# Optimization experiments

Hardware: AMD Instinct MI355X
Metric: run time of the kernel (lower is better)

Reference implementation:

```python
import jax, jax.numpy as jnp
import numpy as np

DIM, DK, DV = 1024, 128, 128

def setup_inputs() -> dict:
    key = jax.random.key(0)
    ks = jax.random.split(key, 7)
    X = jax.random.normal(ks[0], (4, 4096, DIM), dtype=jnp.float32)
    s = DIM ** -0.5
    Wq = jax.random.normal(ks[1], (DIM, DK), dtype=jnp.float32) * s
    bq = jnp.zeros((DK,), dtype=jnp.float32)
    Wk = jax.random.normal(ks[2], (DIM, DK), dtype=jnp.float32) * s
    bk = jnp.zeros((DK,), dtype=jnp.float32)
    Wv = jax.random.normal(ks[3], (DIM, DV), dtype=jnp.float32) * s
    bv = jnp.zeros((DV,), dtype=jnp.float32)
    return {"X": X, "Wq": Wq, "bq": bq, "Wk": Wk, "bk": bk, "Wv": Wv, "bv": bv}

def reference(X, Wq, bq, Wk, bk, Wv, bv):
    scale = DK ** -0.5
    q = X @ Wq + bq              # [B, S, dk]
    k = X @ Wk + bk              # [B, S, dk]
    v = X @ Wv + bv              # [B, S, dv]
    attn = jnp.einsum('bqd,bkd->bqk', q, k) * scale  # [B, S, S]
    attn = jax.nn.softmax(attn, axis=-1)
    return jnp.einsum('bqk,bkd->bqd', attn, v)       # [B, S, dv]
```

## Files before the change

### kernel.cpp

```cpp
#include <hip/hip_runtime.h>

#define NB 4
#define SEQ 4096
#define DIMK 1024
#define DKV 128
#define SCALE 0.08838834764831845f

typedef float  f32x4  __attribute__((ext_vector_type(4)));
typedef float  f32x16 __attribute__((ext_vector_type(16)));
typedef _Float16 f16x8 __attribute__((ext_vector_type(8)));

static __device__ __forceinline__ int pkrtz(float a, float b) {
    auto h = __builtin_amdgcn_cvt_pkrtz(a, b);
    return __builtin_bit_cast(int, h);
}

__global__ void prep_wt(const float* __restrict__ Wq, const float* __restrict__ Wk,
                        const float* __restrict__ Wv, _Float16* __restrict__ WT) {
    int tid = blockIdx.x * 256 + threadIdx.x;
    int n  = tid & 127;
    int k  = (tid >> 7) & 1023;
    int w3 = tid >> 17;
    const float* W = (w3 == 0) ? Wq : (w3 == 1) ? Wk : Wv;
    WT[((size_t)w3 * 128 + n) * 1024 + k] = (_Float16)W[(size_t)k * 128 + n];
}

__global__ __launch_bounds__(256) void qkv_proj(
    const float* __restrict__ X,
    const float* __restrict__ bq, const float* __restrict__ bk, const float* __restrict__ bv,
    const _Float16* __restrict__ WT,
    _Float16* __restrict__ Qh, _Float16* __restrict__ Kh, _Float16* __restrict__ VTh) {

    __shared__ __attribute__((aligned(16))) _Float16 WTs[128 * 40];
    const int t = threadIdx.x;
    const int w = t >> 6, l = t & 63;
    const int lrow = l & 15, lg = l >> 4;
    const int w3   = blockIdx.x % 3;
    const int tile = blockIdx.x / 3;
    const int r0 = tile * 64;

    f32x4 acc[8] = {};
    const float* xrow = X + (size_t)(r0 + w * 16 + lrow) * DIMK;
    const _Float16* Wbase = WT + (size_t)w3 * 128 * 1024;

    float4 xc0 = *(const float4*)(xrow + lg * 8);
    float4 xc1 = *(const float4*)(xrow + lg * 8 + 4);

    for (int k0 = 0; k0 < DIMK; k0 += 32) {
        __syncthreads();
        #pragma unroll
        for (int i = 0; i < 2; ++i) {
            int c = t + 256 * i;
            int row = c >> 2, part = c & 3;
            *(int4*)((char*)WTs + row * 80 + part * 16) =
                *(const int4*)(Wbase + (size_t)row * 1024 + k0 + part * 8);
        }
        float4 xn0, xn1;
        if (k0 + 32 < DIMK) {
            xn0 = *(const float4*)(xrow + k0 + 32 + lg * 8);
            xn1 = *(const float4*)(xrow + k0 + 32 + lg * 8 + 4);
        }
        __syncthreads();
        f16x8 a;
        a[0] = (_Float16)xc0.x; a[1] = (_Float16)xc0.y; a[2] = (_Float16)xc0.z; a[3] = (_Float16)xc0.w;
        a[4] = (_Float16)xc1.x; a[5] = (_Float16)xc1.y; a[6] = (_Float16)xc1.z; a[7] = (_Float16)xc1.w;

        #pragma unroll
        for (int n = 0; n < 8; ++n) {
            f16x8 bf = *(const f16x8*)((const char*)WTs + (n * 16 + lrow) * 80 + lg * 16);
            acc[n] = __builtin_amdgcn_mfma_f32_16x16x32_f16(a, bf, acc[n], 0, 0, 0);
        }
        xc0 = xn0; xc1 = xn1;
    }
    const float* bias = (w3 == 0) ? bq : (w3 == 1) ? bk : bv;
    #pragma unroll
    for (int n = 0; n < 8; ++n) {
        int col = n * 16 + lrow;
        float bv_ = bias[col];
        #pragma unroll
        for (int j = 0; j < 4; ++j) {
            int grow = r0 + w * 16 + lg * 4 + j;
            float val = acc[n][j] + bv_;
            if (w3 == 0) {
                Qh[(size_t)grow * DKV + col] = (_Float16)(val * SCALE);
            } else if (w3 == 1) {
                Kh[(size_t)grow * DKV + col] = (_Float16)val;
            } else {
                int b = grow >> 12, sp = grow & 4095;
                VTh[((size_t)b * DKV + col) * SEQ + sp] = (_Float16)val;
            }
        }
    }
}

__global__ __launch_bounds__(256, 2) void attn_kernel(
    const _Float16* __restrict__ Qh, const _Float16* __restrict__ Kh,
    const _Float16* __restrict__ VTh, float* __restrict__ out) {

    __shared__ __attribute__((aligned(16))) char lds[65536];

    const int t = threadIdx.x;
    const int w = t >> 6, l = t & 63;
    const int lq = l & 31;
    const int hi = l >> 5;

    const int work = (blockIdx.x & 7) * 64 + (blockIdx.x >> 3);
    const int b  = work >> 7;
    const int qt = work & 127;
    const int q0 = qt * 32;

    char* Kw = lds + w * 16384;
    char* Vw = Kw + 8192;

    f16x8 qf[8];
    #pragma unroll
    for (int c = 0; c < 8; ++c)
        qf[c] = *(const f16x8*)(Qh + (size_t)(b * SEQ + q0 + lq) * DKV + c * 16 + hi * 8);

    f32x16 o[4] = {};
    float m = -INFINITY, lsum = 0.f;

    const _Float16* Kbase = Kh + (size_t)(b * SEQ + w * 1024) * DKV;
    const _Float16* Vbase = VTh + (size_t)b * DKV * SEQ + w * 1024;

    const int krow = l >> 4, kpart = l & 15;
    const int vdv  = l >> 2, vp = l & 3;

    {
        int4 kreg[8], vreg[8];
        #pragma unroll
        for (int i = 0; i < 8; ++i)
            kreg[i] = *(const int4*)(Kbase + (size_t)(krow + 4 * i) * DKV + kpart * 8);
        #pragma unroll
        for (int i = 0; i < 8; ++i)
            vreg[i] = *(const int4*)(Vbase + (size_t)(vdv + 16 * i) * SEQ + vp * 8);
        #pragma unroll
        for (int i = 0; i < 8; ++i) {
            int row = krow + 4 * i;
            *(int4*)(Kw + row * 256 + ((kpart * 16) ^ ((row & 15) << 4))) = kreg[i];
        }
        #pragma unroll
        for (int i = 0; i < 8; ++i) {
            int dv = vdv + 16 * i;
            *(int4*)(Vw + dv * 64 + ((vp ^ ((dv >> 1) & 3)) * 16)) = vreg[i];
        }
    }

    for (int kt = 0; kt < 32; ++kt) {
        const int kn = ((kt + 1) & 31) * 32;
        int4 kreg[8], vreg[8];
        #pragma unroll
        for (int i = 0; i < 8; ++i)
            kreg[i] = *(const int4*)(Kbase + (size_t)(kn + krow + 4 * i) * DKV + kpart * 8);
        #pragma unroll
        for (int i = 0; i < 8; ++i)
            vreg[i] = *(const int4*)(Vbase + (size_t)(vdv + 16 * i) * SEQ + kn + vp * 8);

        asm volatile("s_waitcnt lgkmcnt(0)" ::: "memory");
        __builtin_amdgcn_sched_barrier(0);

        f32x16 s = {};
        #pragma unroll
        for (int c = 0; c < 8; ++c) {
            f16x8 kf = *(const f16x8*)(Kw + lq * 256 +
                                       (((2 * c + hi) * 16) ^ ((lq & 15) << 4)));
            s = __builtin_amdgcn_mfma_f32_32x32x16_f16(kf, qf[c], s, 0, 0, 0);
        }

        float tm = -INFINITY;
        #pragma unroll
        for (int r = 0; r < 16; ++r) tm = fmaxf(tm, s[r]);
        tm = fmaxf(tm, __shfl_xor(tm, 32));

        if (__any(tm > m + 8.f)) {
            float mnew = fmaxf(m, tm);
            float corr = __expf(m - mnew);
            m = mnew;
            lsum *= corr;
            #pragma unroll
            for (int dvt = 0; dvt < 4; ++dvt) o[dvt] *= corr;
        }
        float ts = 0.f;
        #pragma unroll
        for (int r = 0; r < 16; ++r) { s[r] = __expf(s[r] - m); ts += s[r]; }
        ts += __shfl_xor(ts, 32);
        lsum += ts;

        int wv[8];
        #pragma unroll
        for (int i = 0; i < 8; ++i) wv[i] = pkrtz(s[2 * i], s[2 * i + 1]);

        #pragma unroll
        for (int s_ = 0; s_ < 2; ++s_) {
            const int base = s_ * 4;
            int x0 = __shfl_xor(wv[base + 0], 32);
            int x1 = __shfl_xor(wv[base + 1], 32);
            int x2 = __shfl_xor(wv[base + 2], 32);
            int x3 = __shfl_xor(wv[base + 3], 32);
            union { int i[4]; f16x8 v; } bu;
            bu.i[0] = hi ? x2 : wv[base + 0];
            bu.i[1] = hi ? x3 : wv[base + 1];
            bu.i[2] = hi ? wv[base + 2] : x0;
            bu.i[3] = hi ? wv[base + 3] : x1;
            #pragma unroll
            for (int dvt = 0; dvt < 4; ++dvt) {
                int rv = dvt * 32 + lq;
                f16x8 vf = *(const f16x8*)(Vw + rv * 64 +
                                           (((s_ * 2 + hi) ^ ((rv >> 1) & 3)) * 16));
                o[dvt] = __builtin_amdgcn_mfma_f32_32x32x16_f16(vf, bu.v, o[dvt], 0, 0, 0);
            }
        }

        #pragma unroll
        for (int i = 0; i < 8; ++i) {
            int row = krow + 4 * i;
            *(int4*)(Kw + row * 256 + ((kpart * 16) ^ ((row & 15) << 4))) = kreg[i];
        }
        #pragma unroll
        for (int i = 0; i < 8; ++i) {
            int dv = vdv + 16 * i;
            *(int4*)(Vw + dv * 64 + ((vp ^ ((dv >> 1) & 3)) * 16)) = vreg[i];
        }
    }

    float* obuf  = (float*)lds;
    float* mlbuf = (float*)(lds + 49152);

    __syncthreads();
    if (w == 1 || w == 3) {
        int sb = (w == 3);
        #pragma unroll
        for (int dvt = 0; dvt < 4; ++dvt)
            #pragma unroll
            for (int r = 0; r < 16; ++r)
                obuf[sb * 4096 + (dvt * 16 + r) * 64 + l] = o[dvt][r];
        if (l < 32) {
            mlbuf[sb * 64 + l * 2 + 0] = m;
            mlbuf[sb * 64 + l * 2 + 1] = lsum;
        }
    }
    __syncthreads();
    if (w == 0 || w == 2) {
        int sb = (w == 2);
        float mo  = mlbuf[sb * 64 + lq * 2 + 0];
        float lo_ = mlbuf[sb * 64 + lq * 2 + 1];
        float mn = fmaxf(m, mo);
        float ca = __expf(m - mn);
        float cb = __expf(mo - mn);
        m = mn;
        lsum = lsum * ca + lo_ * cb;
        #pragma unroll
        for (int dvt = 0; dvt < 4; ++dvt)
            #pragma unroll
            for (int r = 0; r < 16; ++r)
                o[dvt][r] = o[dvt][r] * ca + obuf[sb * 4096 + (dvt * 16 + r) * 64 + l] * cb;
    }
    __syncthreads();
    if (w == 2) {
        #pragma unroll
        for (int dvt = 0; dvt < 4; ++dvt)
            #pragma unroll
            for (int r = 0; r < 16; ++r)
                obuf[(dvt * 16 + r) * 64 + l] = o[dvt][r];
        if (l < 32) {
            mlbuf[l * 2 + 0] = m;
            mlbuf[l * 2 + 1] = lsum;
        }
    }
    __syncthreads();
    if (w == 0) {
        float mo  = mlbuf[lq * 2 + 0];
        float lo_ = mlbuf[lq * 2 + 1];
        float mn = fmaxf(m, mo);
        float ca = __expf(m - mn);
        float cb = __expf(mo - mn);
        float rl = 1.0f / (lsum * ca + lo_ * cb);
        #pragma unroll
        for (int dvt = 0; dvt < 4; ++dvt)
            #pragma unroll
            for (int r = 0; r < 16; ++r)
                o[dvt][r] = (o[dvt][r] * ca + obuf[(dvt * 16 + r) * 64 + l] * cb) * rl;
    }
    __syncthreads();
    float* tbuf = (float*)lds;
    if (w == 0) {
        #pragma unroll
        for (int dvt = 0; dvt < 4; ++dvt)
            #pragma unroll
            for (int r = 0; r < 16; ++r) {
                int dv = dvt * 32 + (r & 3) + 8 * (r >> 2) + 4 * hi;
                tbuf[lq * 132 + dv] = o[dvt][r];
            }
    }
    __syncthreads();
    const size_t obase = (size_t)(b * SEQ + qt * 32) * DKV;
    int row = t >> 3, c0 = (t & 7) * 16;
    #pragma unroll
    for (int i = 0; i < 4; ++i) {
        float4 v = *(const float4*)(tbuf + row * 132 + c0 + i * 4);
        *(float4*)(out + obase + row * 128 + c0 + i * 4) = v;
    }
}

extern "C" void kernel_launch(void* const* d_in, const int* in_sizes, int n_in,
                              void* d_out, int out_size, void* d_ws, size_t ws_size,
                              hipStream_t stream) {
    const float* X  = (const float*)d_in[0];
    const float* Wq = (const float*)d_in[1];
    const float* bq = (const float*)d_in[2];
    const float* Wk = (const float*)d_in[3];
    const float* bk = (const float*)d_in[4];
    const float* Wv = (const float*)d_in[5];
    const float* bv = (const float*)d_in[6];
    float* out = (float*)d_out;

    const size_t nqe = (size_t)NB * SEQ * DKV;
    _Float16* Qh  = (_Float16*)d_ws;
    _Float16* Kh  = Qh  + nqe;
    _Float16* VTh = Kh  + nqe;
    _Float16* WTh = VTh + nqe;

    prep_wt<<<(3 * 1024 * 128) / 256, 256, 0, stream>>>(Wq, Wk, Wv, WTh);
    qkv_proj<<<(NB * SEQ / 64) * 3, 256, 0, stream>>>(X, bq, bk, bv, WTh, Qh, Kh, VTh);
    attn_kernel<<<NB * 128, 256, 0, stream>>>(Qh, Kh, VTh, out);
}
```

Baseline: 124.6 us.

## Double-buffer weight tiles in QKV projection and split attention score accumulation chains

The QKV projection now stages weight tiles of 64 k-values into a double-buffered LDS array, prefetching the next tile into registers while MFMAs run on the current one. This halves the number of iterations and uses one barrier per iteration instead of two. The attention kernel splits the QK^T MFMA accumulation into two independent chains and replaces the serial max and sum reductions with tree reductions to shorten dependency latency. In exchange it uses more LDS and registers in qkv_proj, and it sets a launch bound of two blocks per unit.

```diff
diff --git a/kernel.cpp b/kernel.cpp
--- a/kernel.cpp
+++ b/kernel.cpp
@@ -25,13 +25,13 @@
     WT[((size_t)w3 * 128 + n) * 1024 + k] = (_Float16)W[(size_t)k * 128 + n];
 }
 
-__global__ __launch_bounds__(256) void qkv_proj(
+__global__ __launch_bounds__(256, 2) void qkv_proj(
     const float* __restrict__ X,
     const float* __restrict__ bq, const float* __restrict__ bk, const float* __restrict__ bv,
     const _Float16* __restrict__ WT,
     _Float16* __restrict__ Qh, _Float16* __restrict__ Kh, _Float16* __restrict__ VTh) {
 
-    __shared__ __attribute__((aligned(16))) _Float16 WTs[128 * 40];
+    __shared__ __attribute__((aligned(16))) char WTs[2][128 * 144];
     const int t = threadIdx.x;
     const int w = t >> 6, l = t & 63;
     const int lrow = l & 15, lg = l >> 4;
@@ -43,35 +43,55 @@
     const float* xrow = X + (size_t)(r0 + w * 16 + lrow) * DIMK;
     const _Float16* Wbase = WT + (size_t)w3 * 128 * 1024;
 
+    const int srow = t >> 3, spart = t & 7;
+
+    {
+        int4 wreg[4];
+        #pragma unroll
+        for (int i = 0; i < 4; ++i)
+            wreg[i] = *(const int4*)(Wbase + (size_t)(srow + 32 * i) * 1024 + spart * 8);
+        #pragma unroll
+        for (int i = 0; i < 4; ++i)
+            *(int4*)(WTs[0] + (srow + 32 * i) * 144 + spart * 16) = wreg[i];
+    }
     float4 xc0 = *(const float4*)(xrow + lg * 8);
     float4 xc1 = *(const float4*)(xrow + lg * 8 + 4);
-
-    for (int k0 = 0; k0 < DIMK; k0 += 32) {
+    float4 xc2 = *(const float4*)(xrow + 32 + lg * 8);
+    float4 xc3 = *(const float4*)(xrow + 32 + lg * 8 + 4);
+    __syncthreads();
+
+    for (int kt = 0; kt < 16; ++kt) {
+        const int cur = kt & 1;
+        const int k0n = ((kt + 1) & 15) * 64;
+        float4 xn0 = *(const float4*)(xrow + k0n + lg * 8);
+        float4 xn1 = *(const float4*)(xrow + k0n + lg * 8 + 4);
+        float4 xn2 = *(const float4*)(xrow + k0n + 32 + lg * 8);
+        float4 xn3 = *(const float4*)(xrow + k0n + 32 + lg * 8 + 4);
+        int4 wreg[4];
+        #pragma unroll
+        for (int i = 0; i < 4; ++i)
+            wreg[i] = *(const int4*)(Wbase + (size_t)(srow + 32 * i) * 1024 + k0n + spart * 8);
+
+        #pragma unroll
+        for (int kk = 0; kk < 2; ++kk) {
+            f16x8 a;
+            float4 u = kk ? xc2 : xc0, v = kk ? xc3 : xc1;
+            a[0] = (_Float16)u.x; a[1] = (_Float16)u.y; a[2] = (_Float16)u.z; a[3] = (_Float16)u.w;
+            a[4] = (_Float16)v.x; a[5] = (_Float16)v.y; a[6] = (_Float16)v.z; a[7] = (_Float16)v.w;
+            #pragma unroll
+            for (int n = 0; n < 8; ++n) {
+                f16x8 bf = *(const f16x8*)(WTs[cur] + (n * 16 + lrow) * 144 +
+                                           kk * 64 + lg * 16);
+                acc[n] = __builtin_amdgcn_mfma_f32_16x16x32_f16(a, bf, acc[n], 0, 0, 0);
+            }
+        }
+        #pragma unroll
+        for (int i = 0; i < 4; ++i)
+            *(int4*)(WTs[cur ^ 1] + (srow + 32 * i) * 144 + spart * 16) = wreg[i];
         __syncthreads();
-        #pragma unroll
-        for (int i = 0; i < 2; ++i) {
-            int c = t + 256 * i;
-            int row = c >> 2, part = c & 3;
-            *(int4*)((char*)WTs + row * 80 + part * 16) =
-                *(const int4*)(Wbase + (size_t)row * 1024 + k0 + part * 8);
-        }
-        float4 xn0, xn1;
-        if (k0 + 32 < DIMK) {
-            xn0 = *(const float4*)(xrow + k0 + 32 + lg * 8);
-            xn1 = *(const float4*)(xrow + k0 + 32 + lg * 8 + 4);
-        }
-        __syncthreads();
-        f16x8 a;
-        a[0] = (_Float16)xc0.x; a[1] = (_Float16)xc0.y; a[2] = (_Float16)xc0.z; a[3] = (_Float16)xc0.w;
-        a[4] = (_Float16)xc1.x; a[5] = (_Float16)xc1.y; a[6] = (_Float16)xc1.z; a[7] = (_Float16)xc1.w;
-
-        #pragma unroll
-        for (int n = 0; n < 8; ++n) {
-            f16x8 bf = *(const f16x8*)((const char*)WTs + (n * 16 + lrow) * 80 + lg * 16);
-            acc[n] = __builtin_amdgcn_mfma_f32_16x16x32_f16(a, bf, acc[n], 0, 0, 0);
-        }
-        xc0 = xn0; xc1 = xn1;
-    }
+        xc0 = xn0; xc1 = xn1; xc2 = xn2; xc3 = xn3;
+    }
+
     const float* bias = (w3 == 0) ? bq : (w3 == 1) ? bk : bv;
     #pragma unroll
     for (int n = 0; n < 8; ++n) {
@@ -159,17 +179,26 @@
         asm volatile("s_waitcnt lgkmcnt(0)" ::: "memory");
         __builtin_amdgcn_sched_barrier(0);
 
-        f32x16 s = {};
-        #pragma unroll
-        for (int c = 0; c < 8; ++c) {
-            f16x8 kf = *(const f16x8*)(Kw + lq * 256 +
-                                       (((2 * c + hi) * 16) ^ ((lq & 15) << 4)));
-            s = __builtin_amdgcn_mfma_f32_32x32x16_f16(kf, qf[c], s, 0, 0, 0);
-        }
-
-        float tm = -INFINITY;
-        #pragma unroll
-        for (int r = 0; r < 16; ++r) tm = fmaxf(tm, s[r]);
+        f32x16 sa = {}, sb = {};
+        #pragma unroll
+        for (int c = 0; c < 4; ++c) {
+            f16x8 kfa = *(const f16x8*)(Kw + lq * 256 +
+                                        (((2 * c + hi) * 16) ^ ((lq & 15) << 4)));
+            f16x8 kfb = *(const f16x8*)(Kw + lq * 256 +
+                                        (((2 * (c + 4) + hi) * 16) ^ ((lq & 15) << 4)));
+            sa = __builtin_amdgcn_mfma_f32_32x32x16_f16(kfa, qf[c], sa, 0, 0, 0);
+            sb = __builtin_amdgcn_mfma_f32_32x32x16_f16(kfb, qf[c + 4], sb, 0, 0, 0);
+        }
+        f32x16 s = sa + sb;
+
+        float red[8];
+        #pragma unroll
+        for (int r = 0; r < 8; ++r) red[r] = fmaxf(s[2 * r], s[2 * r + 1]);
+        #pragma unroll
+        for (int r = 0; r < 4; ++r) red[r] = fmaxf(red[r], red[r + 4]);
+        red[0] = fmaxf(red[0], red[2]);
+        red[1] = fmaxf(red[1], red[3]);
+        float tm = fmaxf(red[0], red[1]);
         tm = fmaxf(tm, __shfl_xor(tm, 32));
 
         if (__any(tm > m + 8.f)) {
@@ -180,9 +209,15 @@
             #pragma unroll
             for (int dvt = 0; dvt < 4; ++dvt) o[dvt] *= corr;
         }
-        float ts = 0.f;
-        #pragma unroll
-        for (int r = 0; r < 16; ++r) { s[r] = __expf(s[r] - m); ts += s[r]; }
+        #pragma unroll
+        for (int r = 0; r < 16; ++r) s[r] = __expf(s[r] - m);
+        float sr[8];
+        #pragma unroll
+        for (int r = 0; r < 8; ++r) sr[r] = s[2 * r] + s[2 * r + 1];
+        #pragma unroll
+        for (int r = 0; r < 4; ++r) sr[r] += sr[r + 4];
+        sr[0] += sr[2]; sr[1] += sr[3];
+        float ts = sr[0] + sr[1];
         ts += __shfl_xor(ts, 32);
         lsum += ts;
 
@@ -228,22 +263,22 @@
 
     __syncthreads();
     if (w == 1 || w == 3) {
-        int sb = (w == 3);
+        int sb_ = (w == 3);
         #pragma unroll
         for (int dvt = 0; dvt < 4; ++dvt)
             #pragma unroll
             for (int r = 0; r < 16; ++r)
-                obuf[sb * 4096 + (dvt * 16 + r) * 64 + l] = o[dvt][r];
+                obuf[sb_ * 4096 + (dvt * 16 + r) * 64 + l] = o[dvt][r];
         if (l < 32) {
-            mlbuf[sb * 64 + l * 2 + 0] = m;
-            mlbuf[sb * 64 + l * 2 + 1] = lsum;
+            mlbuf[sb_ * 64 + l * 2 + 0] = m;
+            mlbuf[sb_ * 64 + l * 2 + 1] = lsum;
         }
     }
     __syncthreads();
     if (w == 0 || w == 2) {
-        int sb = (w == 2);
-        float mo  = mlbuf[sb * 64 + lq * 2 + 0];
-        float lo_ = mlbuf[sb * 64 + lq * 2 + 1];
+        int sb_ = (w == 2);
+        float mo  = mlbuf[sb_ * 64 + lq * 2 + 0];
+        float lo_ = mlbuf[sb_ * 64 + lq * 2 + 1];
         float mn = fmaxf(m, mo);
         float ca = __expf(m - mn);
         float cb = __expf(mo - mn);
@@ -253,7 +288,7 @@
         for (int dvt = 0; dvt < 4; ++dvt)
             #pragma unroll
             for (int r = 0; r < 16; ++r)
-                o[dvt][r] = o[dvt][r] * ca + obuf[sb * 4096 + (dvt * 16 + r) * 64 + l] * cb;
+                o[dvt][r] = o[dvt][r] * ca + obuf[sb_ * 4096 + (dvt * 16 + r) * 64 + l] * cb;
     }
     __syncthreads();
     if (w == 2) {
```

Measured after the change: 119.9 us. 3.7% less time.
